# Performance work log

Hardware: AMD Instinct MI355X
Metric: run time of the kernel (lower is better)

The kernel has to match this reference:

```python
import jax, jax.numpy as jnp
import numpy as np

B, S, D, H, L = 8, 4096, 512, 512, 2


def log_g(x):
    # log of g(x) where g(x) = x + 0.5 for x >= 0 else sigmoid(x)
    return jnp.where(x >= 0, jnp.log(jax.nn.relu(x) + 0.5), -jax.nn.softplus(-x))


def g(x):
    return jnp.where(x >= 0, x + 0.5, jax.nn.sigmoid(x))


def mingru_layer(x, h0, wz, bz, wh, bh):
    """Log-space parallel-scan minGRU layer.
    x: (B,S,Din), h0: (B,1,H) positive (already g-activated).
    wz,wh: (H,Din); bz,bh: (H,). Returns full hidden sequence (B,S,H)."""
    k = jnp.einsum('bsd,hd->bsh', x, wz) + bz          # gate pre-activation
    log_z = -jax.nn.softplus(-k)                        # log sigmoid(k)
    log_coeffs = -jax.nn.softplus(k)                    # log(1 - sigmoid(k))
    log_h_tilde = log_g(jnp.einsum('bsd,hd->bsh', x, wh) + bh)
    log_values = log_z + log_h_tilde                    # log(z * h_tilde)
    log_h0 = jnp.log(h0)                                # (B,1,H)
    # Heinsen associative scan in log space
    a_star = jnp.cumsum(
        jnp.concatenate([jnp.zeros_like(log_h0), log_coeffs], axis=1), axis=1)  # (B,S+1,H)
    log_vals = jnp.concatenate([log_h0, log_values], axis=1)                     # (B,S+1,H)
    log_h = a_star + jax.lax.cumlogsumexp(log_vals - a_star, axis=1)
    return jnp.exp(log_h)[:, 1:]                        # (B,S,H)


def setup_inputs() -> dict:
    key = jax.random.key(0)
    ks = jax.random.split(key, 1 + 4 * L)
    x = jax.random.normal(ks[0], (B, S, D), dtype=jnp.float32)
    inp = {'x': x}
    dims_in = [D] + [H] * (L - 1)
    i = 1
    for l in range(L):
        din = dims_in[l]
        stdv = 1.0 / np.sqrt(din)
        inp[f'wz{l}'] = jax.random.uniform(ks[i], (H, din), minval=-stdv, maxval=stdv); i += 1
        inp[f'bz{l}'] = jax.random.uniform(ks[i], (H,), minval=-stdv, maxval=stdv); i += 1
        inp[f'wh{l}'] = jax.random.uniform(ks[i], (H, din), minval=-stdv, maxval=stdv); i += 1
        inp[f'bh{l}'] = jax.random.uniform(ks[i], (H,), minval=-stdv, maxval=stdv); i += 1
    return inp


def reference(x, wz0, bz0, wh0, bh0, wz1, bz1, wh1, bh1):
    # h is None -> h0 = g(zeros) = 0.5 for every layer
    h0 = jnp.full((B, 1, H), 0.5, dtype=x.dtype)
    params = [(wz0, bz0, wh0, bh0), (wz1, bz1, wh1, bh1)]
    inp = x
    finals = []
    for (wz, bz, wh, bh) in params:
        out = mingru_layer(inp, h0, wz, bz, wh, bh)
        finals.append(out[:, -1:])
        inp = out  # Identity layer transform, no residual, dropout=0
    return out, jnp.stack(finals)  # (B,S,H), (L,B,1,H)
```

## Files before the change

kernel.cpp:

```cpp
#include <hip/hip_runtime.h>
#include <math.h>

#define BB 8
#define SS 4096
#define DD 512
#define HH 512
#define MM (BB*SS)

constexpr int TCH = 64;
constexpr int NC  = SS / TCH;
constexpr int BH  = BB * HH;

constexpr int BM = 128;
constexpr int BN = 64;
constexpr int BK = 64;

typedef short  short8  __attribute__((ext_vector_type(8)));
typedef float  float4v __attribute__((ext_vector_type(4)));

__device__ inline unsigned short f2bf(float f) {
    union { float f; unsigned u; } v; v.f = f;
    unsigned r = v.u + 0x7FFF + ((v.u >> 16) & 1);
    return (unsigned short)(r >> 16);
}
__device__ inline float bf_lo(unsigned u) {
    union { unsigned u; float f; } x; x.u = u << 16; return x.f;
}
__device__ inline float bf_hi(unsigned u) {
    union { unsigned u; float f; } x; x.u = u & 0xffff0000u; return x.f;
}

__device__ inline void async_copy16(const void* g, void* l) {
    __builtin_amdgcn_global_load_lds(
        (const __attribute__((address_space(1))) void*)g,
        (__attribute__((address_space(3))) void*)l, 16, 0, 0);
}

__global__ __launch_bounds__(256)
void conv_bf16(const float* __restrict__ in, short* __restrict__ out) {
    const size_t base = ((size_t)blockIdx.x * 256 + threadIdx.x) * 8;
    float4 a = *(const float4*)(in + base);
    float4 b = *(const float4*)(in + base + 4);
    short8 r;
    r[0] = f2bf(a.x); r[1] = f2bf(a.y); r[2] = f2bf(a.z); r[3] = f2bf(a.w);
    r[4] = f2bf(b.x); r[5] = f2bf(b.y); r[6] = f2bf(b.z); r[7] = f2bf(b.w);
    *(short8*)(out + base) = r;
}

__global__ __launch_bounds__(256)
void conv_bf16_w4(const float* __restrict__ w0, const float* __restrict__ w1,
                  const float* __restrict__ w2, const float* __restrict__ w3,
                  short* __restrict__ out) {
    const float* src = (blockIdx.y == 0) ? w0 : (blockIdx.y == 1) ? w1
                     : (blockIdx.y == 2) ? w2 : w3;
    const size_t base = ((size_t)blockIdx.x * 256 + threadIdx.x) * 8;
    float4 a = *(const float4*)(src + base);
    float4 b = *(const float4*)(src + base + 4);
    short8 r;
    r[0] = f2bf(a.x); r[1] = f2bf(a.y); r[2] = f2bf(a.z); r[3] = f2bf(a.w);
    r[4] = f2bf(b.x); r[5] = f2bf(b.y); r[6] = f2bf(b.z); r[7] = f2bf(b.w);
    *(short8*)(out + (size_t)blockIdx.y * HH * DD + base) = r;
}

__global__ __launch_bounds__(256)
void gemm_gate_mfma(const short* __restrict__ Xg, const short* __restrict__ Wz,
                    const float* __restrict__ bz, const short* __restrict__ Wh,
                    const float* __restrict__ bh, unsigned* __restrict__ AV,
                    float* __restrict__ cA, float* __restrict__ cV)
{
    __shared__ char smem[32768];
    short*    lds    = (short*)smem;
    unsigned* lds_av = (unsigned*)smem;
    constexpr int ZOFF = BM * BK;
    constexpr int HOFF = BM * BK + BN * BK;

    const int t    = threadIdx.x;
    const int wave = t >> 6;
    const int lane = t & 63;
    const int col16 = lane & 15;
    const int quad  = lane >> 4;
    const int wm = wave >> 1;
    const int wn = wave & 1;
    const int m0 = blockIdx.x * BM;
    const int n0 = blockIdx.y * BN;

    float4v accz[4][2], acch[4][2];
    #pragma unroll
    for (int i = 0; i < 4; ++i)
        #pragma unroll
        for (int j = 0; j < 2; ++j) {
            accz[i][j] = (float4v){0.f, 0.f, 0.f, 0.f};
            acch[i][j] = (float4v){0.f, 0.f, 0.f, 0.f};
        }

    const int lr = lane >> 3;
    const int lc = (lane & 7) * 8;

    for (int k0 = 0; k0 < DD; k0 += BK) {
        #pragma unroll
        for (int i = 0; i < 4; ++i) {
            const int r0 = wave * 32 + i * 8;
            async_copy16(Xg + (size_t)(m0 + r0 + lr) * DD + k0 + lc,
                         &lds[r0 * BK]);
        }
        #pragma unroll
        for (int i = 0; i < 2; ++i) {
            const int r0 = wave * 16 + i * 8;
            async_copy16(Wz + (size_t)(n0 + r0 + lr) * DD + k0 + lc,
                         &lds[ZOFF + r0 * BK]);
            async_copy16(Wh + (size_t)(n0 + r0 + lr) * DD + k0 + lc,
                         &lds[HOFF + r0 * BK]);
        }
        __syncthreads();

        #pragma unroll
        for (int kk = 0; kk < 2; ++kk) {
            short8 af[4], bzf[2], bhf[2];
            #pragma unroll
            for (int mi = 0; mi < 4; ++mi)
                af[mi] = *(const short8*)&lds[(wm*64 + mi*16 + col16) * BK + kk*32 + quad*8];
            #pragma unroll
            for (int nj = 0; nj < 2; ++nj) {
                bzf[nj] = *(const short8*)&lds[ZOFF + (wn*32 + nj*16 + col16) * BK + kk*32 + quad*8];
                bhf[nj] = *(const short8*)&lds[HOFF + (wn*32 + nj*16 + col16) * BK + kk*32 + quad*8];
            }
            #pragma unroll
            for (int mi = 0; mi < 4; ++mi)
                #pragma unroll
                for (int nj = 0; nj < 2; ++nj) {
                    accz[mi][nj] = __builtin_amdgcn_mfma_f32_16x16x32_bf16(af[mi], bzf[nj], accz[mi][nj], 0, 0, 0);
                    acch[mi][nj] = __builtin_amdgcn_mfma_f32_16x16x32_bf16(af[mi], bhf[nj], acch[mi][nj], 0, 0, 0);
                }
        }
        __syncthreads();
    }

    #pragma unroll
    for (int nj = 0; nj < 2; ++nj) {
        const int ln = wn*32 + nj*16 + col16;
        const int n  = n0 + ln;
        const float bzn = bz[n], bhn = bh[n];
        #pragma unroll
        for (int mi = 0; mi < 4; ++mi) {
            const int lmb = wm*64 + mi*16 + quad*4;
            #pragma unroll
            for (int reg = 0; reg < 4; ++reg) {
                const float kz = accz[mi][nj][reg] + bzn;
                const float kh = acch[mi][nj][reg] + bhn;
                const float a  = 1.0f / (1.0f + __expf(kz));
                const float ht = (kh >= 0.0f) ? (kh + 0.5f)
                                              : (1.0f / (1.0f + __expf(-kh)));
                const float v  = (1.0f - a) * ht;
                const unsigned pav = ((unsigned)f2bf(v) << 16) | f2bf(a);
                const int lm = lmb + reg;
                AV[(size_t)(m0 + lm) * HH + n] = pav;
                lds_av[lm * 64 + ln] = pav;
            }
        }
    }
    __syncthreads();

    if (t < 128) {
        const int c  = t >> 6;
        const int ln = t & 63;
        float prod = 1.0f, hl = 0.0f;
        #pragma unroll 8
        for (int s = 0; s < TCH; ++s) {
            const unsigned u = lds_av[(c * TCH + s) * 64 + ln];
            const float a = bf_lo(u), v = bf_hi(u);
            hl   = fmaf(a, hl, v);
            prod *= a;
        }
        const int b  = m0 >> 12;
        const int cg = ((m0 & 4095) >> 6) + c;
        const size_t ci = (size_t)cg * BH + b * HH + (n0 + ln);
        cA[ci] = prod;
        cV[ci] = hl;
    }
}

__global__ __launch_bounds__(256)
void scan_carry(const float* __restrict__ cA, const float* __restrict__ cV,
                float* __restrict__ hstart, float* __restrict__ finals)
{
    const int ch = blockIdx.x * 256 + threadIdx.x;
    float carry = 0.5f;
    for (int c = 0; c < NC; ++c) {
        const size_t ci = (size_t)c * BH + ch;
        hstart[ci] = carry;
        carry = fmaf(cA[ci], carry, cV[ci]);
    }
    finals[ch] = carry;
}

__global__ __launch_bounds__(256)
void scan_apply_f32(const unsigned* __restrict__ AV,
                    const float* __restrict__ hstart, float* __restrict__ out)
{
    const int h = blockIdx.x * 256 + threadIdx.x;
    const int b = blockIdx.y;
    const int c = blockIdx.z;
    float hcur = hstart[(size_t)c * BH + b * HH + h];
    size_t base = ((size_t)(b * SS + c * TCH)) * HH + h;
    for (int tt = 0; tt < TCH; ++tt) {
        const unsigned u = AV[base];
        hcur = fmaf(bf_lo(u), hcur, bf_hi(u));
        out[base] = hcur;
        base += HH;
    }
}

__global__ __launch_bounds__(256)
void scan_apply_bf16(const unsigned* __restrict__ AV,
                     const float* __restrict__ hstart, short* __restrict__ out)
{
    const int h = blockIdx.x * 256 + threadIdx.x;
    const int b = blockIdx.y;
    const int c = blockIdx.z;
    float hcur = hstart[(size_t)c * BH + b * HH + h];
    size_t base = ((size_t)(b * SS + c * TCH)) * HH + h;
    for (int tt = 0; tt < TCH; ++tt) {
        const unsigned u = AV[base];
        hcur = fmaf(bf_lo(u), hcur, bf_hi(u));
        out[base] = (short)f2bf(hcur);
        base += HH;
    }
}

extern "C" void kernel_launch(void* const* d_in, const int* in_sizes, int n_in,
                              void* d_out, int out_size, void* d_ws, size_t ws_size,
                              hipStream_t stream)
{
    const float* x   = (const float*)d_in[0];
    const float* wz0 = (const float*)d_in[1];
    const float* bz0 = (const float*)d_in[2];
    const float* wh0 = (const float*)d_in[3];
    const float* bh0 = (const float*)d_in[4];
    const float* wz1 = (const float*)d_in[5];
    const float* bz1 = (const float*)d_in[6];
    const float* wh1 = (const float*)d_in[7];
    const float* bh1 = (const float*)d_in[8];

    float* out    = (float*)d_out;
    float* finals = out + (size_t)MM * HH;

    unsigned* AV  = (unsigned*)d_ws;
    short* Xbf    = (short*)(AV + (size_t)MM * HH);
    short* Wbf    = Xbf + (size_t)MM * DD;
    float* cA     = (float*)(Wbf + (size_t)4 * HH * DD);
    float* cV     = cA + (size_t)NC * BH;
    float* hstart = cV + (size_t)NC * BH;

    short* Wz0 = Wbf;
    short* Wh0 = Wbf + (size_t)1 * HH * DD;
    short* Wz1 = Wbf + (size_t)2 * HH * DD;
    short* Wh1 = Wbf + (size_t)3 * HH * DD;

    const dim3 gg(MM / BM, HH / BN);
    const dim3 gs(HH / 256, BB, NC);

    conv_bf16   <<<MM * DD / 8 / 256, 256, 0, stream>>>(x, Xbf);
    conv_bf16_w4<<<dim3(HH * DD / 8 / 256, 4), 256, 0, stream>>>(wz0, wh0, wz1, wh1, Wbf);

    gemm_gate_mfma <<<gg, 256, 0, stream>>>(Xbf, Wz0, bz0, Wh0, bh0, AV, cA, cV);
    scan_carry     <<<BH / 256, 256, 0, stream>>>(cA, cV, hstart, finals);
    scan_apply_bf16<<<gs, 256, 0, stream>>>(AV, hstart, Xbf);

    gemm_gate_mfma <<<gg, 256, 0, stream>>>(Xbf, Wz1, bz1, Wh1, bh1, AV, cA, cV);
    scan_carry     <<<BH / 256, 256, 0, stream>>>(cA, cV, hstart, finals + BH);
    scan_apply_f32 <<<gs, 256, 0, stream>>>(AV, hstart, out);
}
```

Before: 339.8 us.

## Fold chunk-carry scan into apply kernels and vectorize AV stores via LDS

Removes the separate serial scan_carry kernel. Each apply block now recomputes its starting hidden state by folding all preceding chunk summaries, which are packed as float2. The GEMM epilogue also stages the packed a/v values in LDS and writes AV to global memory with coalesced 16-byte stores instead of scattered 4-byte stores. This saves two launches and the serial 64-step carry pass, at the cost of redundant prefix work that grows with chunk index, up to 63 steps per block.

```diff
diff --git a/kernel.cpp b/kernel.cpp
--- a/kernel.cpp
+++ b/kernel.cpp
@@ -66,7 +66,7 @@
 void gemm_gate_mfma(const short* __restrict__ Xg, const short* __restrict__ Wz,
                     const float* __restrict__ bz, const short* __restrict__ Wh,
                     const float* __restrict__ bh, unsigned* __restrict__ AV,
-                    float* __restrict__ cA, float* __restrict__ cV)
+                    float2* __restrict__ cAV)
 {
     __shared__ char smem[32768];
     short*    lds    = (short*)smem;
@@ -151,14 +151,22 @@
                 const float ht = (kh >= 0.0f) ? (kh + 0.5f)
                                               : (1.0f / (1.0f + __expf(-kh)));
                 const float v  = (1.0f - a) * ht;
-                const unsigned pav = ((unsigned)f2bf(v) << 16) | f2bf(a);
-                const int lm = lmb + reg;
-                AV[(size_t)(m0 + lm) * HH + n] = pav;
-                lds_av[lm * 64 + ln] = pav;
+                lds_av[(lmb + reg) * 64 + ln] = ((unsigned)f2bf(v) << 16) | f2bf(a);
             }
         }
     }
     __syncthreads();
+
+    {
+        const int row0 = t >> 4;
+        const int col  = (t & 15) * 4;
+        #pragma unroll
+        for (int i = 0; i < 8; ++i) {
+            const int row = row0 + i * 16;
+            const uint4 u = *(const uint4*)&lds_av[row * 64 + col];
+            *(uint4*)&AV[(size_t)(m0 + row) * HH + n0 + col] = u;
+        }
+    }
 
     if (t < 128) {
         const int c  = t >> 6;
@@ -173,34 +181,24 @@
         }
         const int b  = m0 >> 12;
         const int cg = ((m0 & 4095) >> 6) + c;
-        const size_t ci = (size_t)cg * BH + b * HH + (n0 + ln);
-        cA[ci] = prod;
-        cV[ci] = hl;
-    }
-}
-
-__global__ __launch_bounds__(256)
-void scan_carry(const float* __restrict__ cA, const float* __restrict__ cV,
-                float* __restrict__ hstart, float* __restrict__ finals)
-{
-    const int ch = blockIdx.x * 256 + threadIdx.x;
-    float carry = 0.5f;
-    for (int c = 0; c < NC; ++c) {
-        const size_t ci = (size_t)c * BH + ch;
-        hstart[ci] = carry;
-        carry = fmaf(cA[ci], carry, cV[ci]);
-    }
-    finals[ch] = carry;
+        cAV[(size_t)cg * BH + b * HH + (n0 + ln)] = make_float2(prod, hl);
+    }
 }
 
 __global__ __launch_bounds__(256)
 void scan_apply_f32(const unsigned* __restrict__ AV,
-                    const float* __restrict__ hstart, float* __restrict__ out)
+                    const float2* __restrict__ cAV,
+                    float* __restrict__ out, float* __restrict__ finals)
 {
     const int h = blockIdx.x * 256 + threadIdx.x;
     const int b = blockIdx.y;
     const int c = blockIdx.z;
-    float hcur = hstart[(size_t)c * BH + b * HH + h];
+    const int ch = b * HH + h;
+    float hcur = 0.5f;
+    for (int cp = 0; cp < c; ++cp) {
+        const float2 s = cAV[(size_t)cp * BH + ch];
+        hcur = fmaf(s.x, hcur, s.y);
+    }
     size_t base = ((size_t)(b * SS + c * TCH)) * HH + h;
     for (int tt = 0; tt < TCH; ++tt) {
         const unsigned u = AV[base];
@@ -208,16 +206,23 @@
         out[base] = hcur;
         base += HH;
     }
+    if (c == NC - 1) finals[ch] = hcur;
 }
 
 __global__ __launch_bounds__(256)
 void scan_apply_bf16(const unsigned* __restrict__ AV,
-                     const float* __restrict__ hstart, short* __restrict__ out)
+                     const float2* __restrict__ cAV,
+                     short* __restrict__ out, float* __restrict__ finals)
 {
     const int h = blockIdx.x * 256 + threadIdx.x;
     const int b = blockIdx.y;
     const int c = blockIdx.z;
-    float hcur = hstart[(size_t)c * BH + b * HH + h];
+    const int ch = b * HH + h;
+    float hcur = 0.5f;
+    for (int cp = 0; cp < c; ++cp) {
+        const float2 s = cAV[(size_t)cp * BH + ch];
+        hcur = fmaf(s.x, hcur, s.y);
+    }
     size_t base = ((size_t)(b * SS + c * TCH)) * HH + h;
     for (int tt = 0; tt < TCH; ++tt) {
         const unsigned u = AV[base];
@@ -225,6 +230,7 @@
         out[base] = (short)f2bf(hcur);
         base += HH;
     }
+    if (c == NC - 1) finals[ch] = hcur;
 }
 
 extern "C" void kernel_launch(void* const* d_in, const int* in_sizes, int n_in,
@@ -247,9 +253,7 @@
     unsigned* AV  = (unsigned*)d_ws;
     short* Xbf    = (short*)(AV + (size_t)MM * HH);
     short* Wbf    = Xbf + (size_t)MM * DD;
-    float* cA     = (float*)(Wbf + (size_t)4 * HH * DD);
-    float* cV     = cA + (size_t)NC * BH;
-    float* hstart = cV + (size_t)NC * BH;
+    float2* cAV   = (float2*)(Wbf + (size_t)4 * HH * DD);
 
     short* Wz0 = Wbf;
     short* Wh0 = Wbf + (size_t)1 * HH * DD;
@@ -262,11 +266,9 @@
     conv_bf16   <<<MM * DD / 8 / 256, 256, 0, stream>>>(x, Xbf);
     conv_bf16_w4<<<dim3(HH * DD / 8 / 256, 4), 256, 0, stream>>>(wz0, wh0, wz1, wh1, Wbf);
 
-    gemm_gate_mfma <<<gg, 256, 0, stream>>>(Xbf, Wz0, bz0, Wh0, bh0, AV, cA, cV);
-    scan_carry     <<<BH / 256, 256, 0, stream>>>(cA, cV, hstart, finals);
-    scan_apply_bf16<<<gs, 256, 0, stream>>>(AV, hstart, Xbf);
-
-    gemm_gate_mfma <<<gg, 256, 0, stream>>>(Xbf, Wz1, bz1, Wh1, bh1, AV, cA, cV);
-    scan_carry     <<<BH / 256, 256, 0, stream>>>(cA, cV, hstart, finals + BH);
-    scan_apply_f32 <<<gs, 256, 0, stream>>>(AV, hstart, out);
-}
+    gemm_gate_mfma <<<gg, 256, 0, stream>>>(Xbf, Wz0, bz0, Wh0, bh0, AV, cAV);
+    scan_apply_bf16<<<gs, 256, 0, stream>>>(AV, cAV, Xbf, finals);
+
+    gemm_gate_mfma <<<gg, 256, 0, stream>>>(Xbf, Wz1, bz1, Wh1, bh1, AV, cAV);
+    scan_apply_f32 <<<gs, 256, 0, stream>>>(AV, cAV, out, finals + BH);
+}
```

After: 332.4 us. -2.2%, faster.
